# Performance work log

Hardware: AMD Instinct MI355X
Metric: run time of the kernel (lower is better)

## Reference

```python
import jax, jax.numpy as jnp
import numpy as np

B, H, S, D = 2, 16, 2048, 64
DILATION_RATE = 2

def dilated_global_mask(seq_len: int, dilation_rate: int) -> jnp.ndarray:
    # mask[i, j] = 1 if |i - j| % dilation_rate == 0 else 0  -> [S, S] float32
    i = jnp.arange(seq_len)[:, None]
    j = jnp.arange(seq_len)[None, :]
    return ((jnp.abs(i - j) % dilation_rate) == 0).astype(jnp.float32)

def setup_inputs() -> dict:
    key = jax.random.key(0)
    kq, kk, kv = jax.random.split(key, 3)
    queries = jax.random.normal(kq, (B, H, S, D), dtype=jnp.float32)
    keys = jax.random.normal(kk, (B, H, S, D), dtype=jnp.float32)
    values = jax.random.normal(kv, (B, H, S, D), dtype=jnp.float32)
    return {"queries": queries, "keys": keys, "values": values}

def reference(queries, keys, values):
    depth = queries.shape[-1]
    # scores: [B, H, S, S]
    scores = jnp.einsum("bhqd,bhkd->bhqk", queries, keys)
    scores = scores / jnp.sqrt(jnp.asarray(depth, dtype=jnp.float32))
    gmask = dilated_global_mask(keys.shape[-2], DILATION_RATE)  # [S, S]
    # NOTE: multiplicative masking (masked scores become 0, not -inf), as in source
    masked_scores = scores * gmask
    attention_probs = jax.nn.softmax(masked_scores, axis=-1)
    # dropout is identity at inference (training=None)
    out = jnp.einsum("bhqk,bhkd->bhqd", attention_probs, values)
    return out
```

## Files before the change

### kernel.cpp

```cpp
#include <hip/hip_runtime.h>
#include <hip/hip_bf16.h>


#define B_   2
#define H_   16
#define S_   2048
#define D_   64
#define SP_  1024
#define BQ   64
#define BK   64
#define NKT  (SP_ / BK)

#define QSCALE 0.180336884f

#if __has_builtin(__builtin_amdgcn_exp2f)
#define EXP2(x) __builtin_amdgcn_exp2f(x)
#else
#define EXP2(x) exp2f(x)
#endif

typedef __bf16 bf16x8 __attribute__((ext_vector_type(8)));
typedef __bf16 bf16x4 __attribute__((ext_vector_type(4)));
typedef float  f32x4  __attribute__((ext_vector_type(4)));
typedef short  s16x4  __attribute__((ext_vector_type(4)));

static __device__ __forceinline__ f32x4 mfma16(bf16x4 a, bf16x4 b, f32x4 c) {
    return __builtin_amdgcn_mfma_f32_16x16x16bf16_1k(
        __builtin_bit_cast(s16x4, a), __builtin_bit_cast(s16x4, b), c, 0, 0, 0);
}

#define KSW(r, c8) ((((c8) ^ ((r) & 7)) << 3))

__global__ __launch_bounds__(1024) void vsum_kernel(const float* __restrict__ V,
                                                    float* __restrict__ vs) {
    const int bp  = blockIdx.x;
    const int bh  = bp >> 1;
    const int par = bp & 1;
    const int d   = threadIdx.x & 63;
    const int rg  = threadIdx.x >> 6;
    const float* Vb = V + (size_t)bh * S_ * D_;
    float s = 0.f;
    for (int r = rg; r < SP_; r += 16)
        s += Vb[(size_t)(par + 2 * r) * D_ + d];
    __shared__ float red[16][64];
    red[rg][d] = s;
    __syncthreads();
    if (rg == 0) {
        float t = 0.f;
        #pragma unroll
        for (int i = 0; i < 16; ++i) t += red[i][d];
        vs[(size_t)bp * 64 + d] = t;
    }
}

__global__ __launch_bounds__(256, 4) void attn_kernel(const float* __restrict__ Q,
                                                      const float* __restrict__ K,
                                                      const float* __restrict__ V,
                                                      const float* __restrict__ vs,
                                                      float* __restrict__ out) {
    const int bh  = blockIdx.x;
    const int par = blockIdx.y;
    const int qt  = blockIdx.z;
    const int tid  = threadIdx.x;
    const int lane = tid & 63;
    const int wave = tid >> 6;
    const int l15  = lane & 15;
    const int quad = lane >> 4;

    __shared__ __align__(16) char arena[32768];
    __bf16 (*kbuf)[BK][64] = (__bf16 (*)[BK][64])arena;
    __bf16 (*vbuf)[D_][64] = (__bf16 (*)[D_][64])(arena + 16384);

    const size_t base = (size_t)bh * S_ * D_;
    const float* Qb = Q + base;
    const float* Kb = K + base;
    const float* Vb = V + base;

    bf16x8 qf[2];
    {
        const int qrow = qt * BQ + wave * 16 + l15;
        const float* qsrc = Qb + (size_t)(par + 2 * qrow) * D_ + quad * 8;
        #pragma unroll
        for (int ks = 0; ks < 2; ++ks) {
            const float4 a = *(const float4*)(qsrc + ks * 32);
            const float4 b = *(const float4*)(qsrc + ks * 32 + 4);
            bf16x8 w;
            w[0] = (__bf16)(a.x * QSCALE); w[1] = (__bf16)(a.y * QSCALE);
            w[2] = (__bf16)(a.z * QSCALE); w[3] = (__bf16)(a.w * QSCALE);
            w[4] = (__bf16)(b.x * QSCALE); w[5] = (__bf16)(b.y * QSCALE);
            w[6] = (__bf16)(b.z * QSCALE); w[7] = (__bf16)(b.w * QSCALE);
            qf[ks] = w;
        }
    }

    const int kr0 = tid >> 3;
    const int kc8 = tid & 7;

    float4 pka[2], pkb[2];
    float  pv[16];

    auto issue_loads = [&](int kt) {
        #pragma unroll
        for (int i = 0; i < 2; ++i) {
            const int r = i * 32 + kr0;
            const float* ksrc = Kb + (size_t)(par + 2 * (kt * BK + r)) * D_ + kc8 * 8;
            pka[i] = *(const float4*)ksrc;
            pkb[i] = *(const float4*)(ksrc + 4);
        }
        #pragma unroll
        for (int i = 0; i < 2; ++i) {
            const int c = wave + 4 * i;
            const float* vsrc = Vb + (size_t)(par + 2 * (kt * BK + c * 8)) * D_ + lane;
            #pragma unroll
            for (int j = 0; j < 8; ++j)
                pv[i * 8 + j] = vsrc[(size_t)(2 * j) * D_];
        }
    };

    auto stage = [&](int buf) {
        #pragma unroll
        for (int i = 0; i < 2; ++i) {
            const int r = i * 32 + kr0;
            bf16x8 w;
            w[0] = (__bf16)pka[i].x; w[1] = (__bf16)pka[i].y;
            w[2] = (__bf16)pka[i].z; w[3] = (__bf16)pka[i].w;
            w[4] = (__bf16)pkb[i].x; w[5] = (__bf16)pkb[i].y;
            w[6] = (__bf16)pkb[i].z; w[7] = (__bf16)pkb[i].w;
            *(bf16x8*)&kbuf[buf][r][KSW(r, kc8)] = w;
        }
        #pragma unroll
        for (int i = 0; i < 2; ++i) {
            const int c = wave + 4 * i;
            bf16x8 w;
            #pragma unroll
            for (int j = 0; j < 8; ++j) w[j] = (__bf16)pv[i * 8 + j];
            *(bf16x8*)&vbuf[buf][lane][KSW(lane, c)] = w;
        }
    };

    issue_loads(0);
    stage(0);
    __syncthreads();

    f32x4 acc[4];
    #pragma unroll
    for (int dt = 0; dt < 4; ++dt) acc[dt] = (f32x4){0.f, 0.f, 0.f, 0.f};
    float l_acc = 0.f;

    for (int kt = 0; kt < NKT; ++kt) {
        const int cur = kt & 1;
        const bool pf = (kt + 1 < NKT);

        if (pf) issue_loads(kt + 1);

        const __bf16 (*kb)[64] = kbuf[cur];
        const __bf16 (*vb)[64] = vbuf[cur];

        bf16x8 ka[2][4];
        #pragma unroll
        for (int ks = 0; ks < 2; ++ks)
            #pragma unroll
            for (int kt4 = 0; kt4 < 4; ++kt4) {
                const int R = kt4 * 16 + l15;
                ka[ks][kt4] = *(const bf16x8*)&kb[R][KSW(R, ks * 4 + quad)];
            }
        bf16x4 va[4][4];
        #pragma unroll
        for (int dt = 0; dt < 4; ++dt) {
            const int R = dt * 16 + l15;
            const int ro = R & 7;
            #pragma unroll
            for (int kt4 = 0; kt4 < 4; ++kt4) {
                const int ch = (kt4 * 2 + (quad >> 1)) ^ ro;
                va[kt4][dt] = *(const bf16x4*)&vb[R][ch * 8 + (quad & 1) * 4];
            }
        }

        f32x4 st[4];
        #pragma unroll
        for (int kt4 = 0; kt4 < 4; ++kt4) st[kt4] = (f32x4){0.f, 0.f, 0.f, 0.f};
        #pragma unroll
        for (int ks = 0; ks < 2; ++ks)
            #pragma unroll
            for (int kt4 = 0; kt4 < 4; ++kt4)
                st[kt4] = __builtin_amdgcn_mfma_f32_16x16x32_bf16(
                    ka[ks][kt4], qf[ks], st[kt4], 0, 0, 0);
        #pragma unroll
        for (int kt4 = 0; kt4 < 4; ++kt4) {
            const float p0 = EXP2(st[kt4][0]);
            const float p1 = EXP2(st[kt4][1]);
            const float p2 = EXP2(st[kt4][2]);
            const float p3 = EXP2(st[kt4][3]);
            l_acc += (p0 + p1) + (p2 + p3);
            bf16x4 pb;
            pb[0] = (__bf16)p0; pb[1] = (__bf16)p1;
            pb[2] = (__bf16)p2; pb[3] = (__bf16)p3;
            #pragma unroll
            for (int dt = 0; dt < 4; ++dt)
                acc[dt] = mfma16(va[kt4][dt], pb, acc[dt]);
        }

        if (pf) stage(1 - cur);
        __syncthreads();
    }

    float Z = l_acc;
    Z += __shfl_xor(Z, 16);
    Z += __shfl_xor(Z, 32);
    const float rz = 1.0f / (Z + 1024.0f);

    const float* vso = vs + ((size_t)(bh * 2 + (1 - par))) * 64;

    float* tw = (float*)arena + wave * (16 * 68);
    #pragma unroll
    for (int dt = 0; dt < 4; ++dt) {
        const f32x4 vs4 = *(const f32x4*)&vso[dt * 16 + quad * 4];
        const f32x4 o = (acc[dt] + vs4) * rz;
        *(f32x4*)&tw[l15 * 68 + dt * 16 + quad * 4] = o;
    }
    #pragma unroll
    for (int i = 0; i < 4; ++i) {
        const int q = i * 4 + quad;
        const f32x4 ov = *(const f32x4*)&tw[q * 68 + l15 * 4];
        const int qg = par + 2 * (qt * BQ + wave * 16 + q);
        *(f32x4*)&out[base + (size_t)qg * D_ + l15 * 4] = ov;
    }
}

extern "C" void kernel_launch(void* const* d_in, const int* in_sizes, int n_in,
                              void* d_out, int out_size, void* d_ws, size_t ws_size,
                              hipStream_t stream) {
    const float* Q = (const float*)d_in[0];
    const float* K = (const float*)d_in[1];
    const float* V = (const float*)d_in[2];
    float* out = (float*)d_out;
    float* vs = (float*)d_ws;
    vsum_kernel<<<dim3(B_ * H_ * 2), dim3(1024), 0, stream>>>(V, vs);
    attn_kernel<<<dim3(B_ * H_, 2, SP_ / BQ), dim3(256), 0, stream>>>(Q, K, V, vs, out);
}
```

Measured before the change: 134.5 us.

## Pre-convert K/V to swizzled bf16 tiles in a prepass kernel

Adds a conversion kernel that reads K and V once, converts them to bf16, writes K in the swizzled tile layout and V transposed per tile, and computes partial V column sums along the way. The attention kernel then streams contiguous 16-byte chunks straight into LDS, with no per-element fp32 loads, strided V gathers or conversions in its inner loop. This removes the redundant fp32 reads and conversions repeated by each of the 16 query-tile blocks. In exchange it adds an extra kernel pass and workspace traffic, and falls back to the old path if the workspace is too small.

```diff
diff --git a/kernel.cpp b/kernel.cpp
--- a/kernel.cpp
+++ b/kernel.cpp
@@ -30,6 +30,242 @@
 }
 
 #define KSW(r, c8) ((((c8) ^ ((r) & 7)) << 3))
+
+__global__ __launch_bounds__(256) void conv_kernel(const float* __restrict__ K,
+                                                   const float* __restrict__ V,
+                                                   __bf16* __restrict__ Kbf,
+                                                   __bf16* __restrict__ Vt,
+                                                   float* __restrict__ vsp) {
+    const int bp  = blockIdx.x;
+    const int kc  = blockIdx.y;
+    const int bh  = bp >> 1;
+    const int par = bp & 1;
+    const int tid = threadIdx.x;
+    const float* Kb = K + (size_t)bh * S_ * D_;
+    const float* Vb = V + (size_t)bh * S_ * D_;
+
+    __shared__ __align__(16) __bf16 vt[64][80];
+    const int row = tid >> 2;
+    const int c0  = (tid & 3) * 16;
+    const int c8  = (tid & 3) * 2;
+
+    float vsum = 0.f;
+    #pragma unroll
+    for (int st2 = 0; st2 < 2; ++st2) {
+        const int ktile = kc * 2 + st2;
+        const int k0 = ktile * 64;
+        {
+            const float* ks = Kb + (size_t)(par + 2 * (k0 + row)) * D_ + c0;
+            const float4 a0 = *(const float4*)(ks);
+            const float4 a1 = *(const float4*)(ks + 4);
+            const float4 a2 = *(const float4*)(ks + 8);
+            const float4 a3 = *(const float4*)(ks + 12);
+            bf16x8 w0, w1;
+            w0[0] = (__bf16)a0.x; w0[1] = (__bf16)a0.y;
+            w0[2] = (__bf16)a0.z; w0[3] = (__bf16)a0.w;
+            w0[4] = (__bf16)a1.x; w0[5] = (__bf16)a1.y;
+            w0[6] = (__bf16)a1.z; w0[7] = (__bf16)a1.w;
+            w1[0] = (__bf16)a2.x; w1[1] = (__bf16)a2.y;
+            w1[2] = (__bf16)a2.z; w1[3] = (__bf16)a2.w;
+            w1[4] = (__bf16)a3.x; w1[5] = (__bf16)a3.y;
+            w1[6] = (__bf16)a3.z; w1[7] = (__bf16)a3.w;
+            __bf16* kdst = Kbf + ((size_t)bp * SP_ + k0 + row) * D_;
+            *(bf16x8*)&kdst[KSW(row, c8)]     = w0;
+            *(bf16x8*)&kdst[KSW(row, c8 + 1)] = w1;
+        }
+        {
+            const float* vsrc = Vb + (size_t)(par + 2 * (k0 + row)) * D_ + c0;
+            const float4 a0 = *(const float4*)(vsrc);
+            const float4 a1 = *(const float4*)(vsrc + 4);
+            const float4 a2 = *(const float4*)(vsrc + 8);
+            const float4 a3 = *(const float4*)(vsrc + 12);
+            bf16x8 w0, w1;
+            w0[0] = (__bf16)a0.x; w0[1] = (__bf16)a0.y;
+            w0[2] = (__bf16)a0.z; w0[3] = (__bf16)a0.w;
+            w0[4] = (__bf16)a1.x; w0[5] = (__bf16)a1.y;
+            w0[6] = (__bf16)a1.z; w0[7] = (__bf16)a1.w;
+            w1[0] = (__bf16)a2.x; w1[1] = (__bf16)a2.y;
+            w1[2] = (__bf16)a2.z; w1[3] = (__bf16)a2.w;
+            w1[4] = (__bf16)a3.x; w1[5] = (__bf16)a3.y;
+            w1[6] = (__bf16)a3.z; w1[7] = (__bf16)a3.w;
+            *(bf16x8*)&vt[row][c0]     = w0;
+            *(bf16x8*)&vt[row][c0 + 8] = w1;
+        }
+        __syncthreads();
+        {
+            const int d = row;
+            #pragma unroll
+            for (int cc2 = 0; cc2 < 2; ++cc2) {
+                const int cc = c8 + cc2;
+                bf16x8 w;
+                float s = 0.f;
+                #pragma unroll
+                for (int j = 0; j < 8; ++j) {
+                    w[j] = vt[cc * 8 + j][d];
+                    s += (float)w[j];
+                }
+                vsum += s;
+                __bf16* vdst = Vt + (((size_t)bp * 16 + ktile) * D_ + d) * 64;
+                *(bf16x8*)&vdst[KSW(d, cc)] = w;
+            }
+        }
+        __syncthreads();
+    }
+    vsum += __shfl_down(vsum, 1);
+    vsum += __shfl_down(vsum, 2);
+    if ((tid & 3) == 0) vsp[((size_t)bp * 8 + blockIdx.y) * 64 + row] = vsum;
+}
+
+__global__ __launch_bounds__(256, 4) void attn3_kernel(const float* __restrict__ Q,
+                                                       const __bf16* __restrict__ Kbf,
+                                                       const __bf16* __restrict__ Vt,
+                                                       const float* __restrict__ vsp,
+                                                       float* __restrict__ out) {
+    const int bh  = blockIdx.x;
+    const int par = blockIdx.y;
+    const int qt  = blockIdx.z;
+    const int bp  = bh * 2 + par;
+    const int tid  = threadIdx.x;
+    const int lane = tid & 63;
+    const int wave = tid >> 6;
+    const int l15  = lane & 15;
+    const int quad = lane >> 4;
+
+    __shared__ __align__(16) char arena[32768];
+    __bf16 (*kbuf)[BK][64] = (__bf16 (*)[BK][64])arena;
+    __bf16 (*vbuf)[D_][64] = (__bf16 (*)[D_][64])(arena + 16384);
+
+    const size_t base = (size_t)bh * S_ * D_;
+
+    bf16x8 qf[2];
+    {
+        const int qrow = qt * BQ + wave * 16 + l15;
+        const float* qsrc = Q + base + (size_t)(par + 2 * qrow) * D_ + quad * 8;
+        #pragma unroll
+        for (int ks = 0; ks < 2; ++ks) {
+            const float4 a = *(const float4*)(qsrc + ks * 32);
+            const float4 b = *(const float4*)(qsrc + ks * 32 + 4);
+            bf16x8 w;
+            w[0] = (__bf16)(a.x * QSCALE); w[1] = (__bf16)(a.y * QSCALE);
+            w[2] = (__bf16)(a.z * QSCALE); w[3] = (__bf16)(a.w * QSCALE);
+            w[4] = (__bf16)(b.x * QSCALE); w[5] = (__bf16)(b.y * QSCALE);
+            w[6] = (__bf16)(b.z * QSCALE); w[7] = (__bf16)(b.w * QSCALE);
+            qf[ks] = w;
+        }
+    }
+
+    const uint4* Kt4 = (const uint4*)(Kbf + (size_t)bp * SP_ * D_);
+    const uint4* Vt4 = (const uint4*)(Vt  + (size_t)bp * SP_ * D_);
+    uint4 sk0, sk1, sv0, sv1;
+
+    auto issue_loads = [&](int kt) {
+        const int o = kt * 512 + tid;
+        sk0 = Kt4[o]; sk1 = Kt4[o + 256];
+        sv0 = Vt4[o]; sv1 = Vt4[o + 256];
+    };
+    auto stage = [&](int buf) {
+        uint4* kd = (uint4*)kbuf[buf];
+        uint4* vd = (uint4*)vbuf[buf];
+        kd[tid] = sk0; kd[tid + 256] = sk1;
+        vd[tid] = sv0; vd[tid + 256] = sv1;
+    };
+
+    issue_loads(0);
+    stage(0);
+    __syncthreads();
+
+    f32x4 acc[4];
+    #pragma unroll
+    for (int dt = 0; dt < 4; ++dt) acc[dt] = (f32x4){0.f, 0.f, 0.f, 0.f};
+    float l_acc = 0.f;
+
+    for (int kt = 0; kt < NKT; ++kt) {
+        const int cur = kt & 1;
+        const bool pf = (kt + 1 < NKT);
+
+        if (pf) issue_loads(kt + 1);
+
+        const __bf16 (*kb)[64] = kbuf[cur];
+        const __bf16 (*vb)[64] = vbuf[cur];
+
+        bf16x8 ka[2][4];
+        #pragma unroll
+        for (int ks = 0; ks < 2; ++ks)
+            #pragma unroll
+            for (int kt4 = 0; kt4 < 4; ++kt4) {
+                const int R = kt4 * 16 + l15;
+                ka[ks][kt4] = *(const bf16x8*)&kb[R][KSW(R, ks * 4 + quad)];
+            }
+        bf16x4 va[4][4];
+        #pragma unroll
+        for (int dt = 0; dt < 4; ++dt) {
+            const int R = dt * 16 + l15;
+            const int ro = R & 7;
+            #pragma unroll
+            for (int kt4 = 0; kt4 < 4; ++kt4) {
+                const int ch = (kt4 * 2 + (quad >> 1)) ^ ro;
+                va[kt4][dt] = *(const bf16x4*)&vb[R][ch * 8 + (quad & 1) * 4];
+            }
+        }
+
+        f32x4 st[4];
+        #pragma unroll
+        for (int kt4 = 0; kt4 < 4; ++kt4) st[kt4] = (f32x4){0.f, 0.f, 0.f, 0.f};
+        #pragma unroll
+        for (int ks = 0; ks < 2; ++ks)
+            #pragma unroll
+            for (int kt4 = 0; kt4 < 4; ++kt4)
+                st[kt4] = __builtin_amdgcn_mfma_f32_16x16x32_bf16(
+                    ka[ks][kt4], qf[ks], st[kt4], 0, 0, 0);
+        #pragma unroll
+        for (int kt4 = 0; kt4 < 4; ++kt4) {
+            const float p0 = EXP2(st[kt4][0]);
+            const float p1 = EXP2(st[kt4][1]);
+            const float p2 = EXP2(st[kt4][2]);
+            const float p3 = EXP2(st[kt4][3]);
+            l_acc += (p0 + p1) + (p2 + p3);
+            bf16x4 pb;
+            pb[0] = (__bf16)p0; pb[1] = (__bf16)p1;
+            pb[2] = (__bf16)p2; pb[3] = (__bf16)p3;
+            #pragma unroll
+            for (int dt = 0; dt < 4; ++dt)
+                acc[dt] = mfma16(va[kt4][dt], pb, acc[dt]);
+        }
+
+        if (pf) stage(1 - cur);
+        __syncthreads();
+    }
+
+    float Z = l_acc;
+    Z += __shfl_xor(Z, 16);
+    Z += __shfl_xor(Z, 32);
+    const float rz = 1.0f / (Z + 1024.0f);
+
+    const float* vsb = vsp + (size_t)(bh * 2 + (1 - par)) * 8 * 64;
+    f32x4 vs4[4];
+    #pragma unroll
+    for (int dt = 0; dt < 4; ++dt) {
+        f32x4 s = (f32x4){0.f, 0.f, 0.f, 0.f};
+        #pragma unroll
+        for (int kc = 0; kc < 8; ++kc)
+            s += *(const f32x4*)&vsb[kc * 64 + dt * 16 + quad * 4];
+        vs4[dt] = s;
+    }
+
+    float* tw = (float*)arena + wave * (16 * 68);
+    #pragma unroll
+    for (int dt = 0; dt < 4; ++dt) {
+        const f32x4 o = (acc[dt] + vs4[dt]) * rz;
+        *(f32x4*)&tw[l15 * 68 + dt * 16 + quad * 4] = o;
+    }
+    #pragma unroll
+    for (int i = 0; i < 4; ++i) {
+        const int q = i * 4 + quad;
+        const f32x4 ov = *(const f32x4*)&tw[q * 68 + l15 * 4];
+        const int qg = par + 2 * (qt * BQ + wave * 16 + q);
+        *(f32x4*)&out[base + (size_t)qg * D_ + l15 * 4] = ov;
+    }
+}
 
 __global__ __launch_bounds__(1024) void vsum_kernel(const float* __restrict__ V,
                                                     float* __restrict__ vs) {
@@ -53,11 +289,11 @@
     }
 }
 
-__global__ __launch_bounds__(256, 4) void attn_kernel(const float* __restrict__ Q,
-                                                      const float* __restrict__ K,
-                                                      const float* __restrict__ V,
-                                                      const float* __restrict__ vs,
-                                                      float* __restrict__ out) {
+__global__ __launch_bounds__(256, 4) void attn_fb_kernel(const float* __restrict__ Q,
+                                                         const float* __restrict__ K,
+                                                         const float* __restrict__ V,
+                                                         const float* __restrict__ vs,
+                                                         float* __restrict__ out) {
     const int bh  = blockIdx.x;
     const int par = blockIdx.y;
     const int qt  = blockIdx.z;
@@ -95,7 +331,6 @@
 
     const int kr0 = tid >> 3;
     const int kc8 = tid & 7;
-
     float4 pka[2], pkb[2];
     float  pv[16];
 
@@ -116,7 +351,6 @@
                 pv[i * 8 + j] = vsrc[(size_t)(2 * j) * D_];
         }
     };
-
     auto stage = [&](int buf) {
         #pragma unroll
         for (int i = 0; i < 2; ++i) {
@@ -150,7 +384,6 @@
     for (int kt = 0; kt < NKT; ++kt) {
         const int cur = kt & 1;
         const bool pf = (kt + 1 < NKT);
-
         if (pf) issue_loads(kt + 1);
 
         const __bf16 (*kb)[64] = kbuf[cur];
@@ -208,7 +441,6 @@
     Z += __shfl_xor(Z, 16);
     Z += __shfl_xor(Z, 32);
     const float rz = 1.0f / (Z + 1024.0f);
-
     const float* vso = vs + ((size_t)(bh * 2 + (1 - par))) * 64;
 
     float* tw = (float*)arena + wave * (16 * 68);
@@ -234,7 +466,22 @@
     const float* K = (const float*)d_in[1];
     const float* V = (const float*)d_in[2];
     float* out = (float*)d_out;
-    float* vs = (float*)d_ws;
-    vsum_kernel<<<dim3(B_ * H_ * 2), dim3(1024), 0, stream>>>(V, vs);
-    attn_kernel<<<dim3(B_ * H_, 2, SP_ / BQ), dim3(256), 0, stream>>>(Q, K, V, vs, out);
-}
+
+    const size_t KBF_BYTES = (size_t)64 * SP_ * D_ * sizeof(__bf16);
+    const size_t VSP_BYTES = (size_t)64 * 8 * 64 * sizeof(float);
+    const size_t need = 2 * KBF_BYTES + VSP_BYTES;
+
+    if (ws_size >= need) {
+        __bf16* Kbf = (__bf16*)d_ws;
+        __bf16* Vt  = (__bf16*)((char*)d_ws + KBF_BYTES);
+        float*  vsp = (float*)((char*)d_ws + 2 * KBF_BYTES);
+        conv_kernel<<<dim3(64, 8), dim3(256), 0, stream>>>(K, V, Kbf, Vt, vsp);
+        attn3_kernel<<<dim3(B_ * H_, 2, SP_ / BQ), dim3(256), 0, stream>>>(
+            Q, Kbf, Vt, vsp, out);
+    } else {
+        float* vsn = (float*)d_ws;
+        vsum_kernel<<<dim3(B_ * H_ * 2), dim3(1024), 0, stream>>>(V, vsn);
+        attn_fb_kernel<<<dim3(B_ * H_, 2, SP_ / BQ), dim3(256), 0, stream>>>(
+            Q, K, V, vsn, out);
+    }
+}
```

Result: faster. 125.1 us (-7.0%).

## Precompute fragment-ordered bf16 K/V and drop LDS staging in attention

Applied to the files above, without the earlier changes.

Adds a pre-pass kernel that converts the dilated K and V rows to bf16 in the exact MFMA fragment order and writes per-tile V column sums. A new attention kernel then loads these fragments straight from global memory into registers with double buffering, with no LDS staging or barriers in the main loop. It also doubles the query tile per block to 128 and remaps block indices for locality. The cost is an extra kernel launch, extra workspace traffic and higher register pressure at lower occupancy. The old path remains as a fallback when the workspace is too small.

```diff
diff --git a/kernel.cpp b/kernel.cpp
--- a/kernel.cpp
+++ b/kernel.cpp
@@ -7,7 +7,8 @@
 #define S_   2048
 #define D_   64
 #define SP_  1024
-#define BQ   64
+#define BQ   128
+#define FBQ  64
 #define BK   64
 #define NKT  (SP_ / BK)
 
@@ -30,6 +31,208 @@
 }
 
 #define KSW(r, c8) ((((c8) ^ ((r) & 7)) << 3))
+
+__global__ __launch_bounds__(256) void convf_kernel(const float* __restrict__ K,
+                                                    const float* __restrict__ V,
+                                                    __bf16* __restrict__ Kf,
+                                                    __bf16* __restrict__ Vf,
+                                                    float* __restrict__ vpp) {
+    const int bp  = blockIdx.x;
+    const int kt  = blockIdx.y;
+    const int bh  = bp >> 1;
+    const int par = bp & 1;
+    const int tid  = threadIdx.x;
+    const int lane = tid & 63;
+    const int w    = tid >> 6;
+    const int l15  = lane & 15;
+    const int quad = lane >> 4;
+    const float* Kb = K + (size_t)bh * S_ * D_;
+    const float* Vb = V + (size_t)bh * S_ * D_;
+
+    #pragma unroll
+    for (int i = 0; i < 2; ++i) {
+        const int f   = w * 2 + i;
+        const int ks  = f >> 2;
+        const int kt4 = f & 3;
+        const int key = kt * 64 + kt4 * 16 + l15;
+        const float* src = Kb + (size_t)(par + 2 * key) * D_ + (ks * 4 + quad) * 8;
+        const float4 a = *(const float4*)src;
+        const float4 b = *(const float4*)(src + 4);
+        bf16x8 wv;
+        wv[0] = (__bf16)a.x; wv[1] = (__bf16)a.y;
+        wv[2] = (__bf16)a.z; wv[3] = (__bf16)a.w;
+        wv[4] = (__bf16)b.x; wv[5] = (__bf16)b.y;
+        wv[6] = (__bf16)b.z; wv[7] = (__bf16)b.w;
+        *(bf16x8*)&Kf[(((size_t)bp * NKT + kt) * 8 + f) * 512 + lane * 8] = wv;
+    }
+
+    float ps[4];
+    #pragma unroll
+    for (int dt = 0; dt < 4; ++dt) {
+        const int d = dt * 16 + l15;
+        bf16x4 vv;
+        float s = 0.f;
+        #pragma unroll
+        for (int j = 0; j < 4; ++j) {
+            const int key = kt * 64 + w * 16 + quad * 4 + j;
+            const float x = Vb[(size_t)(par + 2 * key) * D_ + d];
+            vv[j] = (__bf16)x;
+            s += x;
+        }
+        ps[dt] = s;
+        *(bf16x4*)&Vf[(((size_t)bp * NKT + kt) * 16 + (w * 4 + dt)) * 256 + lane * 4] = vv;
+    }
+
+    __shared__ float red[4][4][16];
+    #pragma unroll
+    for (int dt = 0; dt < 4; ++dt) {
+        float s = ps[dt];
+        s += __shfl_xor(s, 16);
+        s += __shfl_xor(s, 32);
+        if (lane < 16) red[w][dt][l15] = s;
+    }
+    __syncthreads();
+    if (tid < 64) {
+        const int dt = tid >> 4, p = tid & 15;
+        vpp[((size_t)bp * NKT + kt) * 64 + tid] =
+            (red[0][dt][p] + red[1][dt][p]) + (red[2][dt][p] + red[3][dt][p]);
+    }
+}
+
+__global__ __launch_bounds__(256, 2) void attn4_kernel(const float* __restrict__ Q,
+                                                       const __bf16* __restrict__ Kf,
+                                                       const __bf16* __restrict__ Vf,
+                                                       const float* __restrict__ vpp,
+                                                       float* __restrict__ out) {
+    const int h  = blockIdx.x;
+    const int L  = (h & 7) * 64 + (h >> 3);
+    const int qt  = L & 7;
+    const int par = (L >> 3) & 1;
+    const int bh  = L >> 4;
+    const int bp  = bh * 2 + par;
+    const int tid  = threadIdx.x;
+    const int lane = tid & 63;
+    const int wave = tid >> 6;
+    const int l15  = lane & 15;
+    const int quad = lane >> 4;
+
+    const size_t base = (size_t)bh * S_ * D_;
+
+    bf16x8 qf[2][2];
+    #pragma unroll
+    for (int qt2 = 0; qt2 < 2; ++qt2) {
+        const int qrow = qt * BQ + wave * 32 + qt2 * 16 + l15;
+        const float* qsrc = Q + base + (size_t)(par + 2 * qrow) * D_ + quad * 8;
+        #pragma unroll
+        for (int ks = 0; ks < 2; ++ks) {
+            const float4 a = *(const float4*)(qsrc + ks * 32);
+            const float4 b = *(const float4*)(qsrc + ks * 32 + 4);
+            bf16x8 w;
+            w[0] = (__bf16)(a.x * QSCALE); w[1] = (__bf16)(a.y * QSCALE);
+            w[2] = (__bf16)(a.z * QSCALE); w[3] = (__bf16)(a.w * QSCALE);
+            w[4] = (__bf16)(b.x * QSCALE); w[5] = (__bf16)(b.y * QSCALE);
+            w[6] = (__bf16)(b.z * QSCALE); w[7] = (__bf16)(b.w * QSCALE);
+            qf[qt2][ks] = w;
+        }
+    }
+
+    const __bf16* Kfb = Kf + (size_t)bp * NKT * 4096;
+    const __bf16* Vfb = Vf + (size_t)bp * NKT * 4096;
+
+    auto LOADK = [&](bf16x8* ka, int kt) {
+        const __bf16* p = Kfb + (size_t)kt * 4096 + lane * 8;
+        #pragma unroll
+        for (int f = 0; f < 8; ++f) ka[f] = *(const bf16x8*)(p + f * 512);
+    };
+    auto LOADV = [&](bf16x4* va, int kt) {
+        const __bf16* p = Vfb + (size_t)kt * 4096 + lane * 4;
+        #pragma unroll
+        for (int g = 0; g < 16; ++g) va[g] = *(const bf16x4*)(p + g * 256);
+    };
+
+    f32x4 acc[2][4];
+    #pragma unroll
+    for (int q2 = 0; q2 < 2; ++q2)
+        #pragma unroll
+        for (int dt = 0; dt < 4; ++dt) acc[q2][dt] = (f32x4){0.f, 0.f, 0.f, 0.f};
+    float l_acc[2] = {0.f, 0.f};
+
+    auto COMPUTE = [&](const bf16x8* ka, const bf16x4* va) {
+        #pragma unroll
+        for (int qt2 = 0; qt2 < 2; ++qt2) {
+            f32x4 st[4];
+            #pragma unroll
+            for (int kt4 = 0; kt4 < 4; ++kt4) st[kt4] = (f32x4){0.f, 0.f, 0.f, 0.f};
+            #pragma unroll
+            for (int ks = 0; ks < 2; ++ks)
+                #pragma unroll
+                for (int kt4 = 0; kt4 < 4; ++kt4)
+                    st[kt4] = __builtin_amdgcn_mfma_f32_16x16x32_bf16(
+                        ka[ks * 4 + kt4], qf[qt2][ks], st[kt4], 0, 0, 0);
+            #pragma unroll
+            for (int kt4 = 0; kt4 < 4; ++kt4) {
+                const float p0 = EXP2(st[kt4][0]);
+                const float p1 = EXP2(st[kt4][1]);
+                const float p2 = EXP2(st[kt4][2]);
+                const float p3 = EXP2(st[kt4][3]);
+                l_acc[qt2] += (p0 + p1) + (p2 + p3);
+                bf16x4 pb;
+                pb[0] = (__bf16)p0; pb[1] = (__bf16)p1;
+                pb[2] = (__bf16)p2; pb[3] = (__bf16)p3;
+                #pragma unroll
+                for (int dt = 0; dt < 4; ++dt)
+                    acc[qt2][dt] = mfma16(va[kt4 * 4 + dt], pb, acc[qt2][dt]);
+            }
+        }
+    };
+
+    bf16x8 kaA[8], kaB[8];
+    bf16x4 vaA[16], vaB[16];
+    LOADK(kaA, 0); LOADV(vaA, 0);
+    for (int kt = 0; kt < NKT; kt += 2) {
+        LOADK(kaB, kt + 1); LOADV(vaB, kt + 1);
+        COMPUTE(kaA, vaA);
+        if (kt + 2 < NKT) { LOADK(kaA, kt + 2); LOADV(vaA, kt + 2); }
+        COMPUTE(kaB, vaB);
+    }
+
+    float rz[2];
+    #pragma unroll
+    for (int qt2 = 0; qt2 < 2; ++qt2) {
+        float Z = l_acc[qt2];
+        Z += __shfl_xor(Z, 16);
+        Z += __shfl_xor(Z, 32);
+        rz[qt2] = 1.0f / (Z + 1024.0f);
+    }
+    const float* vsb = vpp + (size_t)(bh * 2 + (1 - par)) * NKT * 64;
+    f32x4 vs4[4];
+    #pragma unroll
+    for (int dt = 0; dt < 4; ++dt) {
+        f32x4 s = (f32x4){0.f, 0.f, 0.f, 0.f};
+        #pragma unroll
+        for (int kt = 0; kt < NKT; ++kt)
+            s += *(const f32x4*)&vsb[kt * 64 + dt * 16 + quad * 4];
+        vs4[dt] = s;
+    }
+
+    __shared__ __align__(16) float tw_all[4][16 * 68];
+    float* tw = tw_all[wave];
+    #pragma unroll
+    for (int qt2 = 0; qt2 < 2; ++qt2) {
+        #pragma unroll
+        for (int dt = 0; dt < 4; ++dt) {
+            const f32x4 o = (acc[qt2][dt] + vs4[dt]) * rz[qt2];
+            *(f32x4*)&tw[l15 * 68 + dt * 16 + quad * 4] = o;
+        }
+        #pragma unroll
+        for (int i = 0; i < 4; ++i) {
+            const int q = i * 4 + quad;
+            const f32x4 ov = *(const f32x4*)&tw[q * 68 + l15 * 4];
+            const int qg = par + 2 * (qt * BQ + wave * 32 + qt2 * 16 + q);
+            *(f32x4*)&out[base + (size_t)qg * D_ + l15 * 4] = ov;
+        }
+    }
+}
 
 __global__ __launch_bounds__(1024) void vsum_kernel(const float* __restrict__ V,
                                                     float* __restrict__ vs) {
@@ -53,11 +256,11 @@
     }
 }
 
-__global__ __launch_bounds__(256, 4) void attn_kernel(const float* __restrict__ Q,
-                                                      const float* __restrict__ K,
-                                                      const float* __restrict__ V,
-                                                      const float* __restrict__ vs,
-                                                      float* __restrict__ out) {
+__global__ __launch_bounds__(256, 4) void attn_fb_kernel(const float* __restrict__ Q,
+                                                         const float* __restrict__ K,
+                                                         const float* __restrict__ V,
+                                                         const float* __restrict__ vs,
+                                                         float* __restrict__ out) {
     const int bh  = blockIdx.x;
     const int par = blockIdx.y;
     const int qt  = blockIdx.z;
@@ -78,7 +281,7 @@
 
     bf16x8 qf[2];
     {
-        const int qrow = qt * BQ + wave * 16 + l15;
+        const int qrow = qt * FBQ + wave * 16 + l15;
         const float* qsrc = Qb + (size_t)(par + 2 * qrow) * D_ + quad * 8;
         #pragma unroll
         for (int ks = 0; ks < 2; ++ks) {
@@ -95,7 +298,6 @@
 
     const int kr0 = tid >> 3;
     const int kc8 = tid & 7;
-
     float4 pka[2], pkb[2];
     float  pv[16];
 
@@ -116,7 +318,6 @@
                 pv[i * 8 + j] = vsrc[(size_t)(2 * j) * D_];
         }
     };
-
     auto stage = [&](int buf) {
         #pragma unroll
         for (int i = 0; i < 2; ++i) {
@@ -150,7 +351,6 @@
     for (int kt = 0; kt < NKT; ++kt) {
         const int cur = kt & 1;
         const bool pf = (kt + 1 < NKT);
-
         if (pf) issue_loads(kt + 1);
 
         const __bf16 (*kb)[64] = kbuf[cur];
@@ -208,7 +408,6 @@
     Z += __shfl_xor(Z, 16);
     Z += __shfl_xor(Z, 32);
     const float rz = 1.0f / (Z + 1024.0f);
-
     const float* vso = vs + ((size_t)(bh * 2 + (1 - par))) * 64;
 
     float* tw = (float*)arena + wave * (16 * 68);
@@ -222,7 +421,7 @@
     for (int i = 0; i < 4; ++i) {
         const int q = i * 4 + quad;
         const f32x4 ov = *(const f32x4*)&tw[q * 68 + l15 * 4];
-        const int qg = par + 2 * (qt * BQ + wave * 16 + q);
+        const int qg = par + 2 * (qt * FBQ + wave * 16 + q);
         *(f32x4*)&out[base + (size_t)qg * D_ + l15 * 4] = ov;
     }
 }
@@ -234,7 +433,22 @@
     const float* K = (const float*)d_in[1];
     const float* V = (const float*)d_in[2];
     float* out = (float*)d_out;
-    float* vs = (float*)d_ws;
-    vsum_kernel<<<dim3(B_ * H_ * 2), dim3(1024), 0, stream>>>(V, vs);
-    attn_kernel<<<dim3(B_ * H_, 2, SP_ / BQ), dim3(256), 0, stream>>>(Q, K, V, vs, out);
-}
+
+    const size_t KF_BYTES  = (size_t)64 * NKT * 4096 * sizeof(__bf16);
+    const size_t VF_BYTES  = (size_t)64 * NKT * 4096 * sizeof(__bf16);
+    const size_t VPP_BYTES = (size_t)64 * NKT * 64 * sizeof(float);
+    const size_t need = KF_BYTES + VF_BYTES + VPP_BYTES;
+
+    if (ws_size >= need) {
+        __bf16* Kf  = (__bf16*)d_ws;
+        __bf16* Vf  = (__bf16*)((char*)d_ws + KF_BYTES);
+        float*  vpp = (float*)((char*)d_ws + KF_BYTES + VF_BYTES);
+        convf_kernel<<<dim3(64, NKT), dim3(256), 0, stream>>>(K, V, Kf, Vf, vpp);
+        attn4_kernel<<<dim3(512), dim3(256), 0, stream>>>(Q, Kf, Vf, vpp, out);
+    } else {
+        float* vsn = (float*)d_ws;
+        vsum_kernel<<<dim3(B_ * H_ * 2), dim3(1024), 0, stream>>>(V, vsn);
+        attn_fb_kernel<<<dim3(B_ * H_, 2, SP_ / FBQ), dim3(256), 0, stream>>>(
+            Q, K, V, vsn, out);
+    }
+}
```

Result: faster. 128.0 us (-4.9%).
